# Kernel tuning notes

Hardware: AMD Instinct MI355X
Metric: run time of the kernel (lower is better)

The kernel has to match this reference:

```python
import jax, jax.numpy as jnp
import numpy as np


def setup_inputs() -> dict:
    key = jax.random.key(0)
    k1, k2 = jax.random.split(key)
    B, G, P = 64, 4999, 50
    raw_gene_expr = jax.random.normal(k1, (B, G), dtype=jnp.float32)
    # binary pathway membership matrix, mimics torch.randint(0, 2, (P, G)).float()
    pathway_gene_matrix = (jax.random.uniform(k2, (P, G)) < 0.5).astype(jnp.float32)
    return {"raw_gene_expr": raw_gene_expr, "pathway_gene_matrix": pathway_gene_matrix}


def reference(raw_gene_expr, pathway_gene_matrix):
    """Vectorized ssGSEA enrichment (compute_pathway_activations0).

    raw_gene_expr:        [B, G] float
    pathway_gene_matrix:  [P, G] binary float
    returns:              [B, P] signed max-deviation enrichment scores
    """
    B, G = raw_gene_expr.shape
    P = pathway_gene_matrix.shape[0]

    # Sort genes per sample in descending expression order
    order = jnp.argsort(-raw_gene_expr, axis=1)                      # [B, G]
    sorted_expr = jnp.take_along_axis(raw_gene_expr, order, axis=1)  # [B, G]

    # hit[b, p, i] = 1 if gene at sorted position i belongs to pathway p
    hit = (pathway_gene_matrix[:, order] > 0)                        # [P, B, G]
    hit = jnp.transpose(hit, (1, 0, 2)).astype(raw_gene_expr.dtype)  # [B, P, G]

    size = jnp.sum(pathway_gene_matrix > 0, axis=1).astype(raw_gene_expr.dtype)  # [P]

    # Weighted hit increments: |expr|^0.25 over hits, normalized per (sample, pathway)
    w = (jnp.abs(sorted_expr) ** 0.25)[:, None, :] * hit             # [B, P, G]
    s = jnp.sum(w, axis=-1, keepdims=True)
    w = jnp.where(s > 0, w / jnp.where(s > 0, s, 1.0), w)

    cum_hit = jnp.cumsum(w, axis=-1)                                 # [B, P, G]
    denom = jnp.maximum(G - size, 1.0)[None, :, None]                # guard size==G
    cum_miss = jnp.cumsum((1.0 - hit) / denom, axis=-1)              # [B, P, G]

    running = cum_hit - cum_miss                                     # [B, P, G]
    pos = jnp.argmax(jnp.abs(running), axis=-1)                      # [B, P]
    # signed max deviation == running value at the argmax of |running|
    es = jnp.take_along_axis(running, pos[..., None], axis=-1)[..., 0]  # [B, P]
    es = jnp.where(size[None, :] > 0, es, 0.0)
    return es
```

## Files before the change

### kernel.cpp

```cpp
#include <hip/hip_runtime.h>
#include <math.h>

typedef unsigned long long ull;

constexpr int Bc = 64;
constexpr int Gc = 4999;
constexpr int Pc = 50;

constexpr int RUN   = 1024;
constexpr int NRUN  = 5;
constexpr int NPAD  = NRUN * RUN;
constexpr int LPW4  = 21;
constexpr int QSPAN = 64 * LPW4;
constexpr ull PADKEY = 0xFFFFFFFFFFFFFFFFull;

__device__ __forceinline__ ull shfl_xor64(ull v, int lm) {
    int lo = __shfl_xor((int)(unsigned)(v & 0xFFFFFFFFull), lm, 64);
    int hi = __shfl_xor((int)(unsigned)(v >> 32), lm, 64);
    return ((ull)(unsigned)hi << 32) | (unsigned)lo;
}

__global__ __launch_bounds__(512) void chunk_sort(
    const float* __restrict__ expr, const float* __restrict__ pathway,
    ull* __restrict__ runs, ull* __restrict__ pbits, int P, int G)
{
    __shared__ ull key[RUN];
    const int r = blockIdx.x, b = blockIdx.y, tid = threadIdx.x;
    const int base = tid * 2;
    const float* row = expr + (size_t)b * G;

    ull v[2];
#pragma unroll
    for (int o = 0; o < 2; ++o) {
        int i = r * RUN + base + o;
        if (i < G) {
            unsigned u = __float_as_uint(row[i]);
            unsigned m = (u >> 31) ? ~u : (u | 0x80000000u);
            v[o] = ((ull)(~m) << 32) | (unsigned)i;
        } else {
            v[o] = PADKEY;
        }
    }

    for (int kk = 2; kk <= RUN; kk <<= 1) {
        const int j0 = kk >> 1;
        if (j0 >= 128) {
#pragma unroll
            for (int o = 0; o < 2; ++o) key[base + o] = v[o];
            __syncthreads();
            for (int j = j0; j >= 128; j >>= 1) {
                for (int t = tid; t < RUN / 2; t += 512) {
                    int i  = ((t & ~(j - 1)) << 1) | (t & (j - 1));
                    int ix = i | j;
                    ull a = key[i], c = key[ix];
                    bool up = ((i & kk) == 0);
                    if ((a > c) == up) { key[i] = c; key[ix] = a; }
                }
                __syncthreads();
            }
#pragma unroll
            for (int o = 0; o < 2; ++o) v[o] = key[base + o];
        }
        int jstart = (j0 > 64) ? 64 : j0;
        for (int j = jstart; j >= 2; j >>= 1) {
            int lm = j >> 1;
            bool takeMin = (((tid & lm) == 0) == ((base & kk) == 0));
#pragma unroll
            for (int o = 0; o < 2; ++o) {
                ull c = shfl_xor64(v[o], lm);
                ull mn = (v[o] < c) ? v[o] : c;
                ull mx = (v[o] < c) ? c : v[o];
                v[o] = takeMin ? mn : mx;
            }
        }
        {
            bool up = ((base & kk) == 0);
            if ((v[0] > v[1]) == up) { ull t = v[0]; v[0] = v[1]; v[1] = t; }
        }
    }

    ull* dst = runs + ((size_t)b * NRUN + r) * RUN;
#pragma unroll
    for (int o = 0; o < 2; ++o) dst[base + o] = v[o];

    if (r == 0) {
        int g = b * 512 + tid;
        if (g < G) {
            ull m = 0;
#pragma unroll
            for (int p = 0; p < Pc; ++p)
                if (pathway[(size_t)p * G + g] > 0.0f) m |= (1ull << p);
            pbits[g] = m;
        }
    }
}

__global__ __launch_bounds__(1024) void rank_scatter(
    const ull* __restrict__ runs, const ull* __restrict__ pbits,
    float* __restrict__ wqout, ull* __restrict__ pbout, int G)
{
    __shared__ ull runsLDS[NPAD];
    const int rg = blockIdx.x, b = blockIdx.y, tid = threadIdx.x;

    const ull* rowruns = runs + (size_t)b * NPAD;
    for (int i = tid; i < NPAD; i += 1024) runsLDS[i] = rowruns[i];
    __syncthreads();

    const int e = rg * 1024 + tid;
    const ull keyv = runsLDS[e];
    if (keyv == PADKEY) return;

    const int idx = (int)(unsigned)(keyv & 0xFFFFFFFFu);
    const ull pb = pbits[idx];

    const int run = e >> 10;
    int rank = e & 1023;
#pragma unroll
    for (int rr = 0; rr < NRUN; ++rr) {
        if (rr == run) continue;
        const ull* arr = &runsLDS[rr * RUN];
        int pos = 0;
#pragma unroll
        for (int s = RUN; s >= 1; s >>= 1) {
            int np = pos + s;
            if (np <= RUN && arr[np - 1] < keyv) pos = np;
        }
        rank += pos;
    }

    unsigned m = ~((unsigned)(keyv >> 32));
    unsigned absbits = ((m >> 31) ? m : ~m) & 0x7FFFFFFFu;
    float av = __uint_as_float(absbits);
    wqout[(size_t)b * G + rank] = sqrtf(sqrtf(av));
    pbout[(size_t)b * G + rank] = pb;
}

__global__ __launch_bounds__(1024) void es_kernel(
    const float* __restrict__ wq, const ull* __restrict__ pb64,
    float* __restrict__ out, int B, int P, int G)
{
    __shared__ float    swq[Gc];
    __shared__ unsigned sm32[Gc];
    __shared__ double   cSW[4][4][4];
    __shared__ int      cSH[4][4][4];
    __shared__ double   cBV[4][4][4];
    __shared__ double   cBR[4][4][4];

    const int pg = blockIdx.x;
    const int b  = blockIdx.y;
    const int tid = threadIdx.x;
    const int pbeg = pg * 13;
    const int pend = (pbeg + 13 < P) ? (pbeg + 13) : P;

    for (int i = tid; i < G; i += 1024) {
        swq[i]  = wq[(size_t)b * G + i];
        sm32[i] = (unsigned)(pb64[(size_t)b * G + i] >> pbeg);
    }
    __syncthreads();

    const int lane = tid & 63;
    const int w  = tid >> 6;
    const int qg = w >> 2;
    const int h  = w & 3;
    const int sh4 = qg * 4;

    const int lg = h * 64 + lane;
    const int start = lg * LPW4;
    int cnt = G - start;
    cnt = (cnt < 0) ? 0 : ((cnt > LPW4) ? LPW4 : cnt);

    double sw[4] = {0.0, 0.0, 0.0, 0.0};
    int sh[4] = {0, 0, 0, 0};
    for (int k = 0; k < cnt; ++k) {
        int s = start + k;
        unsigned nib = (sm32[s] >> sh4) & 15u;
        double wv = (double)swq[s];
#pragma unroll
        for (int q = 0; q < 4; ++q) {
            if ((nib >> q) & 1u) { sw[q] += wv; sh[q]++; }
        }
    }
#pragma unroll
    for (int q = 0; q < 4; ++q) {
        double s_ = sw[q]; int c_ = sh[q];
#pragma unroll
        for (int off = 1; off < 64; off <<= 1) {
            s_ += __shfl_xor(s_, off, 64);
            c_ += __shfl_xor(c_, off, 64);
        }
        if (lane == 0) { cSW[qg][h][q] = s_; cSH[qg][h][q] = c_; }
    }
    __syncthreads();

    int Qc[4];
#pragma unroll
    for (int hh = 0; hh < 4; ++hh) {
        int c = G - hh * QSPAN;
        Qc[hh] = (c < 0) ? 0 : ((c > QSPAN) ? QSPAN : c);
    }

    double norm[4], inv_denom[4], running[4];
    int shtot[4];
#pragma unroll
    for (int q = 0; q < 4; ++q) {
        double st = 0.0; int ct = 0;
#pragma unroll
        for (int hh = 0; hh < 4; ++hh) { st += cSW[qg][hh][q]; ct += cSH[qg][hh][q]; }
        shtot[q]     = ct;
        norm[q]      = (st > 0.0) ? 1.0 / st : 1.0;
        inv_denom[q] = 1.0 / fmax((double)(G - ct), 1.0);
        double offq = 0.0;
        for (int hh = 0; hh < h; ++hh)
            offq += cSW[qg][hh][q] * norm[q]
                  - (double)(Qc[hh] - cSH[qg][hh][q]) * inv_denom[q];
        double csum = sw[q] * norm[q] - (double)(cnt - sh[q]) * inv_denom[q];
        double x = csum;
#pragma unroll
        for (int off = 1; off < 64; off <<= 1) {
            double vv = __shfl_up(x, off, 64);
            if (lane >= off) x += vv;
        }
        running[q] = x - csum + offq;
    }

    double bestv[4] = {-1.0, -1.0, -1.0, -1.0};
    double bestr[4] = {0.0, 0.0, 0.0, 0.0};
    int besti[4] = {0x7FFFFFFF, 0x7FFFFFFF, 0x7FFFFFFF, 0x7FFFFFFF};
    for (int k = 0; k < cnt; ++k) {
        int s = start + k;
        unsigned nib = (sm32[s] >> sh4) & 15u;
        double wv = (double)swq[s];
#pragma unroll
        for (int q = 0; q < 4; ++q) {
            running[q] += ((nib >> q) & 1u) ? wv * norm[q] : -inv_denom[q];
            double a = fabs(running[q]);
            if (a > bestv[q]) { bestv[q] = a; bestr[q] = running[q]; besti[q] = s; }
        }
    }
#pragma unroll
    for (int q = 0; q < 4; ++q) {
#pragma unroll
        for (int off = 1; off < 64; off <<= 1) {
            double ov  = __shfl_xor(bestv[q], off, 64);
            double orr = __shfl_xor(bestr[q], off, 64);
            int    oi  = __shfl_xor(besti[q], off, 64);
            if (ov > bestv[q] || (ov == bestv[q] && oi < besti[q])) {
                bestv[q] = ov; bestr[q] = orr; besti[q] = oi;
            }
        }
        if (lane == 0) { cBV[qg][h][q] = bestv[q]; cBR[qg][h][q] = bestr[q]; }
    }
    __syncthreads();

    if (h == 0 && lane == 0) {
#pragma unroll
        for (int q = 0; q < 4; ++q) {
            double bv = cBV[qg][0][q];
            double br = cBR[qg][0][q];
#pragma unroll
            for (int hh = 1; hh < 4; ++hh) {
                double v_ = cBV[qg][hh][q];
                if (v_ > bv) { bv = v_; br = cBR[qg][hh][q]; }
            }
            int p = pbeg + sh4 + q;
            if (p < pend)
                out[(size_t)b * P + p] = (shtot[q] > 0) ? (float)br : 0.0f;
        }
    }
}

extern "C" void kernel_launch(void* const* d_in, const int* in_sizes, int n_in,
                              void* d_out, int out_size, void* d_ws, size_t ws_size,
                              hipStream_t stream) {
    const float* expr    = (const float*)d_in[0];
    const float* pathway = (const float*)d_in[1];
    float* out = (float*)d_out;

    char* ws = (char*)d_ws;
    ull*   pbits = (ull*)ws;
    ull*   runs  = (ull*)(ws + 40960);
    float* wqa   = (float*)(ws + 2662400);
    ull*   pb64  = (ull*)(ws + 3942144);

    chunk_sort<<<dim3(NRUN, Bc), dim3(512), 0, stream>>>(
        expr, pathway, runs, pbits, Pc, Gc);
    rank_scatter<<<dim3(NRUN, Bc), dim3(1024), 0, stream>>>(runs, pbits, wqa, pb64, Gc);
    es_kernel<<<dim3(4, Bc), dim3(1024), 0, stream>>>(
        wqa, pb64, out, Bc, Pc, Gc);
}
```

Baseline: 105.5 us.

## Fuse sort, rank scatter and enrichment into one kernel with in-LDS full sort

Replaces the three-kernel pipeline (per-run bitonic sort, merge-rank scatter through global memory, ES scan) with a single kernel per (pathway-group, sample). Each block sorts the whole padded 8192-key row in shared memory, with 8 keys per thread and register-level compare stages. It then writes sorted weights and 13-bit pathway masks into a unioned LDS region and runs the existing ES scan. This removes two launches and the global-memory round trips, but each of the 4 pathway-group blocks redundantly sorts the same sample row, and the sort covers 8192 padded elements.

```diff
diff --git a/kernel.cpp b/kernel.cpp
--- a/kernel.cpp
+++ b/kernel.cpp
@@ -7,9 +7,9 @@
 constexpr int Gc = 4999;
 constexpr int Pc = 50;
 
-constexpr int RUN   = 1024;
-constexpr int NRUN  = 5;
-constexpr int NPAD  = NRUN * RUN;
+constexpr int N8 = 8192;
+constexpr int E  = 8;
+constexpr int T  = 1024;
 constexpr int LPW4  = 21;
 constexpr int QSPAN = 64 * LPW4;
 constexpr ull PADKEY = 0xFFFFFFFFFFFFFFFFull;
@@ -20,19 +20,48 @@
     return ((ull)(unsigned)hi << 32) | (unsigned)lo;
 }
 
-__global__ __launch_bounds__(512) void chunk_sort(
+struct SMem {
+    union U {
+        ull key[N8];
+        struct S {
+            float          swq[5120];
+            unsigned short sm16[5120];
+        } s;
+    } u;
+    unsigned short pbwin[5120];
+    double cSW[4][4][4];
+    int    cSH[4][4][4];
+    double cBV[4][4][4];
+    double cBR[4][4][4];
+};
+
+__global__ __launch_bounds__(1024) void mono_es(
     const float* __restrict__ expr, const float* __restrict__ pathway,
-    ull* __restrict__ runs, ull* __restrict__ pbits, int P, int G)
+    float* __restrict__ out, int B, int P, int G)
 {
-    __shared__ ull key[RUN];
-    const int r = blockIdx.x, b = blockIdx.y, tid = threadIdx.x;
-    const int base = tid * 2;
+    __shared__ SMem sm;
+    const int pg  = blockIdx.x;
+    const int b   = blockIdx.y;
+    const int tid = threadIdx.x;
+    const int pbeg = pg * 13;
+    const int pend = (pbeg + 13 < P) ? (pbeg + 13) : P;
+    const int base = tid * E;
+
+    for (int g = tid; g < G; g += T) {
+        unsigned mask = 0;
+#pragma unroll
+        for (int p = 0; p < 13; ++p) {
+            int pp = pbeg + p;
+            if (pp < Pc && pathway[(size_t)pp * G + g] > 0.0f) mask |= (1u << p);
+        }
+        sm.pbwin[g] = (unsigned short)mask;
+    }
+
     const float* row = expr + (size_t)b * G;
-
-    ull v[2];
-#pragma unroll
-    for (int o = 0; o < 2; ++o) {
-        int i = r * RUN + base + o;
+    ull v[E];
+#pragma unroll
+    for (int o = 0; o < E; ++o) {
+        int i = base + o;
         if (i < G) {
             unsigned u = __float_as_uint(row[i]);
             unsigned m = (u >> 31) ? ~u : (u | 0x80000000u);
@@ -42,119 +71,68 @@
         }
     }
 
-    for (int kk = 2; kk <= RUN; kk <<= 1) {
+    for (int kk = 2; kk <= N8; kk <<= 1) {
         const int j0 = kk >> 1;
-        if (j0 >= 128) {
-#pragma unroll
-            for (int o = 0; o < 2; ++o) key[base + o] = v[o];
+        if (j0 >= 512) {
+#pragma unroll
+            for (int o = 0; o < E; ++o) sm.u.key[base + o] = v[o];
             __syncthreads();
-            for (int j = j0; j >= 128; j >>= 1) {
-                for (int t = tid; t < RUN / 2; t += 512) {
+            for (int j = j0; j >= 512; j >>= 1) {
+#pragma unroll
+                for (int it = 0; it < (N8 / 2) / T; ++it) {
+                    int t  = tid + it * T;
                     int i  = ((t & ~(j - 1)) << 1) | (t & (j - 1));
                     int ix = i | j;
-                    ull a = key[i], c = key[ix];
+                    ull a = sm.u.key[i], c = sm.u.key[ix];
                     bool up = ((i & kk) == 0);
-                    if ((a > c) == up) { key[i] = c; key[ix] = a; }
+                    if ((a > c) == up) { sm.u.key[i] = c; sm.u.key[ix] = a; }
                 }
                 __syncthreads();
             }
 #pragma unroll
-            for (int o = 0; o < 2; ++o) v[o] = key[base + o];
-        }
-        int jstart = (j0 > 64) ? 64 : j0;
-        for (int j = jstart; j >= 2; j >>= 1) {
-            int lm = j >> 1;
+            for (int o = 0; o < E; ++o) v[o] = sm.u.key[base + o];
+        }
+        int jstart = (j0 > 256) ? 256 : j0;
+        for (int j = jstart; j >= E; j >>= 1) {
+            int lm = j >> 3;
             bool takeMin = (((tid & lm) == 0) == ((base & kk) == 0));
 #pragma unroll
-            for (int o = 0; o < 2; ++o) {
+            for (int o = 0; o < E; ++o) {
                 ull c = shfl_xor64(v[o], lm);
                 ull mn = (v[o] < c) ? v[o] : c;
                 ull mx = (v[o] < c) ? c : v[o];
                 v[o] = takeMin ? mn : mx;
             }
         }
-        {
-            bool up = ((base & kk) == 0);
-            if ((v[0] > v[1]) == up) { ull t = v[0]; v[0] = v[1]; v[1] = t; }
-        }
-    }
-
-    ull* dst = runs + ((size_t)b * NRUN + r) * RUN;
-#pragma unroll
-    for (int o = 0; o < 2; ++o) dst[base + o] = v[o];
-
-    if (r == 0) {
-        int g = b * 512 + tid;
-        if (g < G) {
-            ull m = 0;
-#pragma unroll
-            for (int p = 0; p < Pc; ++p)
-                if (pathway[(size_t)p * G + g] > 0.0f) m |= (1ull << p);
-            pbits[g] = m;
-        }
-    }
-}
-
-__global__ __launch_bounds__(1024) void rank_scatter(
-    const ull* __restrict__ runs, const ull* __restrict__ pbits,
-    float* __restrict__ wqout, ull* __restrict__ pbout, int G)
-{
-    __shared__ ull runsLDS[NPAD];
-    const int rg = blockIdx.x, b = blockIdx.y, tid = threadIdx.x;
-
-    const ull* rowruns = runs + (size_t)b * NPAD;
-    for (int i = tid; i < NPAD; i += 1024) runsLDS[i] = rowruns[i];
-    __syncthreads();
-
-    const int e = rg * 1024 + tid;
-    const ull keyv = runsLDS[e];
-    if (keyv == PADKEY) return;
-
-    const int idx = (int)(unsigned)(keyv & 0xFFFFFFFFu);
-    const ull pb = pbits[idx];
-
-    const int run = e >> 10;
-    int rank = e & 1023;
-#pragma unroll
-    for (int rr = 0; rr < NRUN; ++rr) {
-        if (rr == run) continue;
-        const ull* arr = &runsLDS[rr * RUN];
-        int pos = 0;
-#pragma unroll
-        for (int s = RUN; s >= 1; s >>= 1) {
-            int np = pos + s;
-            if (np <= RUN && arr[np - 1] < keyv) pos = np;
-        }
-        rank += pos;
-    }
-
-    unsigned m = ~((unsigned)(keyv >> 32));
-    unsigned absbits = ((m >> 31) ? m : ~m) & 0x7FFFFFFFu;
-    float av = __uint_as_float(absbits);
-    wqout[(size_t)b * G + rank] = sqrtf(sqrtf(av));
-    pbout[(size_t)b * G + rank] = pb;
-}
-
-__global__ __launch_bounds__(1024) void es_kernel(
-    const float* __restrict__ wq, const ull* __restrict__ pb64,
-    float* __restrict__ out, int B, int P, int G)
-{
-    __shared__ float    swq[Gc];
-    __shared__ unsigned sm32[Gc];
-    __shared__ double   cSW[4][4][4];
-    __shared__ int      cSH[4][4][4];
-    __shared__ double   cBV[4][4][4];
-    __shared__ double   cBR[4][4][4];
-
-    const int pg = blockIdx.x;
-    const int b  = blockIdx.y;
-    const int tid = threadIdx.x;
-    const int pbeg = pg * 13;
-    const int pend = (pbeg + 13 < P) ? (pbeg + 13) : P;
-
-    for (int i = tid; i < G; i += 1024) {
-        swq[i]  = wq[(size_t)b * G + i];
-        sm32[i] = (unsigned)(pb64[(size_t)b * G + i] >> pbeg);
+#pragma unroll
+        for (int j = 4; j >= 1; j >>= 1) {
+            if (j < kk) {
+#pragma unroll
+                for (int o = 0; o < E; ++o) {
+                    if ((o & j) == 0) {
+                        bool up = (((base + o) & kk) == 0);
+                        ull a = v[o], c = v[o | j];
+                        if ((a > c) == up) { v[o] = c; v[o | j] = a; }
+                    }
+                }
+            }
+        }
+    }
+
+    __syncthreads();
+
+#pragma unroll
+    for (int o = 0; o < E; ++o) {
+        ull kv = v[o];
+        if (kv != PADKEY) {
+            int pos = base + o;
+            int idx = (int)(unsigned)(kv & 0xFFFFFFFFu);
+            unsigned m = ~((unsigned)(kv >> 32));
+            unsigned absbits = ((m >> 31) ? m : ~m) & 0x7FFFFFFFu;
+            float av = __uint_as_float(absbits);
+            sm.u.s.swq[pos]  = sqrtf(sqrtf(av));
+            sm.u.s.sm16[pos] = sm.pbwin[idx];
+        }
     }
     __syncthreads();
 
@@ -173,8 +151,8 @@
     int sh[4] = {0, 0, 0, 0};
     for (int k = 0; k < cnt; ++k) {
         int s = start + k;
-        unsigned nib = (sm32[s] >> sh4) & 15u;
-        double wv = (double)swq[s];
+        unsigned nib = ((unsigned)sm.u.s.sm16[s] >> sh4) & 15u;
+        double wv = (double)sm.u.s.swq[s];
 #pragma unroll
         for (int q = 0; q < 4; ++q) {
             if ((nib >> q) & 1u) { sw[q] += wv; sh[q]++; }
@@ -188,7 +166,7 @@
             s_ += __shfl_xor(s_, off, 64);
             c_ += __shfl_xor(c_, off, 64);
         }
-        if (lane == 0) { cSW[qg][h][q] = s_; cSH[qg][h][q] = c_; }
+        if (lane == 0) { sm.cSW[qg][h][q] = s_; sm.cSH[qg][h][q] = c_; }
     }
     __syncthreads();
 
@@ -205,14 +183,14 @@
     for (int q = 0; q < 4; ++q) {
         double st = 0.0; int ct = 0;
 #pragma unroll
-        for (int hh = 0; hh < 4; ++hh) { st += cSW[qg][hh][q]; ct += cSH[qg][hh][q]; }
+        for (int hh = 0; hh < 4; ++hh) { st += sm.cSW[qg][hh][q]; ct += sm.cSH[qg][hh][q]; }
         shtot[q]     = ct;
         norm[q]      = (st > 0.0) ? 1.0 / st : 1.0;
         inv_denom[q] = 1.0 / fmax((double)(G - ct), 1.0);
         double offq = 0.0;
         for (int hh = 0; hh < h; ++hh)
-            offq += cSW[qg][hh][q] * norm[q]
-                  - (double)(Qc[hh] - cSH[qg][hh][q]) * inv_denom[q];
+            offq += sm.cSW[qg][hh][q] * norm[q]
+                  - (double)(Qc[hh] - sm.cSH[qg][hh][q]) * inv_denom[q];
         double csum = sw[q] * norm[q] - (double)(cnt - sh[q]) * inv_denom[q];
         double x = csum;
 #pragma unroll
@@ -228,8 +206,8 @@
     int besti[4] = {0x7FFFFFFF, 0x7FFFFFFF, 0x7FFFFFFF, 0x7FFFFFFF};
     for (int k = 0; k < cnt; ++k) {
         int s = start + k;
-        unsigned nib = (sm32[s] >> sh4) & 15u;
-        double wv = (double)swq[s];
+        unsigned nib = ((unsigned)sm.u.s.sm16[s] >> sh4) & 15u;
+        double wv = (double)sm.u.s.swq[s];
 #pragma unroll
         for (int q = 0; q < 4; ++q) {
             running[q] += ((nib >> q) & 1u) ? wv * norm[q] : -inv_denom[q];
@@ -248,19 +226,19 @@
                 bestv[q] = ov; bestr[q] = orr; besti[q] = oi;
             }
         }
-        if (lane == 0) { cBV[qg][h][q] = bestv[q]; cBR[qg][h][q] = bestr[q]; }
+        if (lane == 0) { sm.cBV[qg][h][q] = bestv[q]; sm.cBR[qg][h][q] = bestr[q]; }
     }
     __syncthreads();
 
     if (h == 0 && lane == 0) {
 #pragma unroll
         for (int q = 0; q < 4; ++q) {
-            double bv = cBV[qg][0][q];
-            double br = cBR[qg][0][q];
+            double bv = sm.cBV[qg][0][q];
+            double br = sm.cBR[qg][0][q];
 #pragma unroll
             for (int hh = 1; hh < 4; ++hh) {
-                double v_ = cBV[qg][hh][q];
-                if (v_ > bv) { bv = v_; br = cBR[qg][hh][q]; }
+                double v_ = sm.cBV[qg][hh][q];
+                if (v_ > bv) { bv = v_; br = sm.cBR[qg][hh][q]; }
             }
             int p = pbeg + sh4 + q;
             if (p < pend)
@@ -275,16 +253,8 @@
     const float* expr    = (const float*)d_in[0];
     const float* pathway = (const float*)d_in[1];
     float* out = (float*)d_out;
-
-    char* ws = (char*)d_ws;
-    ull*   pbits = (ull*)ws;
-    ull*   runs  = (ull*)(ws + 40960);
-    float* wqa   = (float*)(ws + 2662400);
-    ull*   pb64  = (ull*)(ws + 3942144);
-
-    chunk_sort<<<dim3(NRUN, Bc), dim3(512), 0, stream>>>(
-        expr, pathway, runs, pbits, Pc, Gc);
-    rank_scatter<<<dim3(NRUN, Bc), dim3(1024), 0, stream>>>(runs, pbits, wqa, pb64, Gc);
-    es_kernel<<<dim3(4, Bc), dim3(1024), 0, stream>>>(
-        wqa, pb64, out, Bc, Pc, Gc);
+    (void)d_ws; (void)ws_size;
+
+    mono_es<<<dim3(4, Bc), dim3(T), 0, stream>>>(
+        expr, pathway, out, Bc, Pc, Gc);
 }
```

Result: slower. 157.7 us (+49.5%).
